# Optimization experiments

Hardware: AMD Instinct MI355X
Metric: run time of the kernel (lower is better)

## Reference

```python
import jax, jax.numpy as jnp
import numpy as np

DIM = 1024
NUM_HEADS = 16
HEAD_DIM = DIM // NUM_HEADS
B, T = 2, 2048


def _rope_tables(seq_len, head_dim, dtype=jnp.float32):
    inv_freq = 1.0 / (10000.0 ** (jnp.arange(0, head_dim, 2, dtype=jnp.float32) / head_dim))
    t = jnp.arange(seq_len, dtype=jnp.float32)
    freqs = jnp.einsum('i,j->ij', t, inv_freq)            # [T, head_dim/2]
    emb = jnp.concatenate((freqs, freqs), axis=-1)         # [T, head_dim]
    return jnp.cos(emb).astype(dtype), jnp.sin(emb).astype(dtype)


def _rotate_half(x):
    x1, x2 = x[..., : x.shape[-1] // 2], x[..., x.shape[-1] // 2 :]
    return jnp.concatenate((-x2, x1), axis=-1)


def setup_inputs() -> dict:
    key = jax.random.key(0)
    ks = jax.random.split(key, 5)
    s = 1.0 / np.sqrt(DIM)
    return {
        'x': jax.random.normal(ks[0], (B, T, DIM), dtype=jnp.float32),
        'w_q': jax.random.normal(ks[1], (DIM, DIM), dtype=jnp.float32) * s,
        'w_k': jax.random.normal(ks[2], (DIM, DIM), dtype=jnp.float32) * s,
        'w_v': jax.random.normal(ks[3], (DIM, DIM), dtype=jnp.float32) * s,
        'w_out': jax.random.normal(ks[4], (DIM, DIM), dtype=jnp.float32) * s,
    }


def reference(x, w_q, w_k, w_v, w_out):
    Bn, Tn, C = x.shape
    scale = HEAD_DIM ** -0.5
    # nn.Linear(bias=False): y = x @ W^T; reshape to [B, H, T, Dh]
    def proj(w):
        y = jnp.einsum('btc,dc->btd', x, w)
        return y.reshape(Bn, Tn, NUM_HEADS, HEAD_DIM).transpose(0, 2, 1, 3)
    q, k, v = proj(w_q), proj(w_k), proj(w_v)
    cos, sin = _rope_tables(Tn, HEAD_DIM, x.dtype)         # [T, Dh], broadcasts over B,H
    q = q * cos + _rotate_half(q) * sin
    k = k * cos + _rotate_half(k) * sin
    attn = jnp.einsum('bhqd,bhkd->bhqk', q, k) * scale     # [B,H,T,T]
    attn = jax.nn.softmax(attn, axis=-1)
    out = jnp.einsum('bhqk,bhkd->bhqd', attn, v)           # [B,H,T,Dh]
    out = out.transpose(0, 2, 1, 3).reshape(Bn, Tn, C)
    return jnp.einsum('btc,dc->btd', out, w_out)
```

## Files before the change

### kernel.cpp

```cpp
#include <hip/hip_runtime.h>


typedef _Float16 f16;
typedef f16 f16x8 __attribute__((ext_vector_type(8)));
typedef __fp16 fp16x2 __attribute__((ext_vector_type(2)));
typedef float f32x4 __attribute__((ext_vector_type(4)));
typedef float f32x16 __attribute__((ext_vector_type(16)));
typedef unsigned int u32;
typedef unsigned short u16;

union V16 { uint4 u; f16x8 h; };

__device__ __forceinline__ float exp2_fast(float x) {
#if __has_builtin(__builtin_amdgcn_exp2f)
  return __builtin_amdgcn_exp2f(x);
#else
  return __expf(x * 0.69314718056f);
#endif
}

__device__ __forceinline__ u32 pkrtz(float a, float b) {
  union { fp16x2 h; u32 u; } cv;
  cv.h = __builtin_amdgcn_cvt_pkrtz(a, b);
  return cv.u;
}

#define PLSWAP(a, b)                                                          \
  asm volatile("s_nop 1\n\tv_permlane32_swap_b32 %0, %1" : "+v"(a), "+v"(b))

#define GLDS(src, dst) __builtin_amdgcn_global_load_lds(                      \
    (const __attribute__((address_space(1))) void*)(const void*)(src),        \
    (__attribute__((address_space(3))) void*)(void*)(dst), 16, 0, 0)

__global__ __launch_bounds__(256) void rope_tables_kernel(float* __restrict__ cosT,
                                                          float* __restrict__ sinT) {
  int i = blockIdx.x * 256 + threadIdx.x;
  int t = i >> 5, j = i & 31;
  float inv = 1.0f / powf(10000.0f, (float)(2 * j) * (1.0f / 64.0f));
  float ang = (float)t * inv;
  double a = (double)ang;
  cosT[i] = (float)cos(a);
  sinT[i] = (float)sin(a);
}

__global__ __launch_bounds__(256)
void cvt5_kernel(const float* __restrict__ x,  const float* __restrict__ wq,
                 const float* __restrict__ wk, const float* __restrict__ wv,
                 const float* __restrict__ wo,
                 f16* __restrict__ xh, f16* __restrict__ W3,
                 f16* __restrict__ woh) {
  int bx = blockIdx.x;
  const float* src; f16* dst; int i;
  if (bx < 4096) {
    src = x; dst = xh; i = bx * 256 + threadIdx.x;
  } else {
    int b = (bx - 4096) >> 10;
    i = ((bx - 4096) & 1023) * 256 + threadIdx.x;
    src = (b == 0) ? wq : (b == 1) ? wk : (b == 2) ? wv : wo;
    dst = (b == 3) ? woh : W3 + (size_t)b * 1048576;
  }
  float4 v = ((const float4*)src)[i];
  union { f16 h[4]; uint2 u; } cv;
  cv.h[0] = (f16)v.x; cv.h[1] = (f16)v.y; cv.h[2] = (f16)v.z; cv.h[3] = (f16)v.w;
  ((uint2*)dst)[i] = cv.u;
}

__global__ __launch_bounds__(256)
void gemm_qkv_kernel(const f16* __restrict__ X,
                     const f16* __restrict__ W3,
                     f16* __restrict__ Qo, f16* __restrict__ Ko,
                     f16* __restrict__ VTo,
                     const float* __restrict__ cosT,
                     const float* __restrict__ sinT) {
  __shared__ u16 lds[2][8192];

  const int tid = threadIdx.x, lane = tid & 63, w = tid >> 6;
  const int c = lane & 15, g = lane >> 4;
  const int m0 = blockIdx.x * 128;
  const int by = blockIdx.y;
  const int wsel = by >> 3, hp = by & 7, h0 = hp * 2;
  const f16* Wb = W3 + (size_t)wsel * (1024 * 1024) + (size_t)hp * 128 * 1024;

  const int n1 = tid, n2 = tid + 256;
  const int r1 = n1 >> 2, gc1 = (n1 & 3) ^ ((n1 >> 3) & 3);
  const int r2 = n2 >> 2, gc2 = (n2 & 3) ^ ((n2 >> 3) & 3);
  const f16* gA1 = X + (size_t)(m0 + r1) * 1024 + gc1 * 8;
  const f16* gA2 = X + (size_t)(m0 + r2) * 1024 + gc2 * 8;
  const f16* gB1 = Wb + (size_t)r1 * 1024 + gc1 * 8;
  const f16* gB2 = Wb + (size_t)r2 * 1024 + gc2 * 8;
  const int dA1 = n1 * 8, dA2 = n2 * 8;
  const int dB1 = 4096 + n1 * 8, dB2 = 4096 + n2 * 8;

  f32x4 acc[2][8];
  const f32x4 zero = {0.f, 0.f, 0.f, 0.f};
#pragma unroll
  for (int mi = 0; mi < 2; ++mi)
#pragma unroll
    for (int ni = 0; ni < 8; ++ni) acc[mi][ni] = zero;

#define STAGE_QKV(buf, kt) do {                                               \
    const int ko = (kt) * 32;                                                 \
    GLDS(gA1 + ko, &lds[buf][dA1]);                                           \
    GLDS(gA2 + ko, &lds[buf][dA2]);                                           \
    GLDS(gB1 + ko, &lds[buf][dB1]);                                           \
    GLDS(gB2 + ko, &lds[buf][dB2]);                                           \
  } while (0)

  const int swz = (g ^ ((c >> 1) & 3)) * 8;

  STAGE_QKV(0, 0);
  __syncthreads();
  for (int kt = 0; kt < 32; ++kt) {
    const int cur = kt & 1;
    if (kt < 31) STAGE_QKV(cur ^ 1, kt + 1);
    V16 a[2], b[8];
#pragma unroll
    for (int mi = 0; mi < 2; ++mi)
      a[mi].u = *(const uint4*)&lds[cur][(w * 32 + mi * 16 + c) * 32 + swz];
#pragma unroll
    for (int ni = 0; ni < 8; ++ni)
      b[ni].u = *(const uint4*)&lds[cur][4096 + (ni * 16 + c) * 32 + swz];
    __builtin_amdgcn_s_setprio(1);
#pragma unroll
    for (int mi = 0; mi < 2; ++mi)
#pragma unroll
      for (int ni = 0; ni < 8; ++ni)
        acc[mi][ni] = __builtin_amdgcn_mfma_f32_16x16x32_f16(a[mi].h, b[ni].h, acc[mi][ni], 0, 0, 0);
    __builtin_amdgcn_s_setprio(0);
    __syncthreads();
  }

  if (wsel < 2) {
    f16* Out = (wsel == 0) ? Qo : Ko;
    const float psc = (wsel == 0) ? 0.18033688f : 1.0f;
#pragma unroll
    for (int mi = 0; mi < 2; ++mi)
#pragma unroll
      for (int r = 0; r < 4; ++r) {
        int m = m0 + w * 32 + mi * 16 + g * 4 + r;
        int bb = m >> 11, t = m & 2047;
        float co0 = cosT[t * 32 + c],      si0 = sinT[t * 32 + c];
        float co1 = cosT[t * 32 + 16 + c], si1 = sinT[t * 32 + 16 + c];
#pragma unroll
        for (int ni = 0; ni < 8; ++ni) {
          int head = h0 + (ni >> 2);
          int d = (ni & 3) * 16 + c;
          float co = (ni & 1) ? co1 : co0;
          float si = (ni & 1) ? si1 : si0;
          float partner = acc[mi][ni ^ 2][r];
          float v = (acc[mi][ni][r] * co + ((d < 32) ? -partner : partner) * si) * psc;
          Out[((size_t)(bb * 16 + head) * 2048 + t) * 64 + d] = (f16)v;
        }
      }
  } else {
    u16* sT = &lds[0][0];
    const int bbv = m0 >> 11;
    const int t0 = (m0 & 2047) + w * 32;
#pragma unroll
    for (int p = 0; p < 2; ++p) {
#pragma unroll
      for (int mi = 0; mi < 2; ++mi)
#pragma unroll
        for (int nn = 0; nn < 4; ++nn)
#pragma unroll
          for (int r = 0; r < 4; ++r) {
            int ni = p * 4 + nn;
            int dl = nn * 16 + c;
            int tl = mi * 16 + g * 4 + r;
            union { f16 h; u16 u; } cv; cv.h = (f16)acc[mi][ni][r];
            sT[w * 2560 + dl * 40 + tl] = cv.u;
          }
      f16* dst = VTo + ((size_t)(bbv * 16 + h0 + p) * 64 + lane) * 2048 + t0;
      const u16* srcp = &sT[w * 2560 + lane * 40];
      *(uint4*)(dst +  0) = *(const uint4*)(srcp +  0);
      *(uint4*)(dst +  8) = *(const uint4*)(srcp +  8);
      *(uint4*)(dst + 16) = *(const uint4*)(srcp + 16);
      *(uint4*)(dst + 24) = *(const uint4*)(srcp + 24);
    }
  }
}

__global__ __launch_bounds__(256)
void gemm_out_kernel(const f16* __restrict__ AH, const f16* __restrict__ BH,
                     float* __restrict__ outF) {
  __shared__ u16 lds[2][6144];

  const int tid = threadIdx.x, lane = tid & 63, w = tid >> 6;
  const int c = lane & 15, g = lane >> 4;
  const int m0 = blockIdx.x * 128, n0 = blockIdx.y * 64;

  const int n1 = tid, n2 = tid + 256;
  const int r1 = n1 >> 2, gc1 = (n1 & 3) ^ ((n1 >> 3) & 3);
  const int r2 = n2 >> 2, gc2 = (n2 & 3) ^ ((n2 >> 3) & 3);
  const f16* gA1 = AH + (size_t)(m0 + r1) * 1024 + gc1 * 8;
  const f16* gA2 = AH + (size_t)(m0 + r2) * 1024 + gc2 * 8;
  const f16* gB1 = BH + (size_t)(n0 + r1) * 1024 + gc1 * 8;
  const int dA1 = n1 * 8, dA2 = n2 * 8;
  const int dB1 = 4096 + n1 * 8;

  f32x4 acc[2][4];
  const f32x4 zero = {0.f, 0.f, 0.f, 0.f};
#pragma unroll
  for (int mi = 0; mi < 2; ++mi)
#pragma unroll
    for (int ni = 0; ni < 4; ++ni) acc[mi][ni] = zero;

#define STAGE_OUT(buf, kt) do {                                               \
    const int ko = (kt) * 32;                                                 \
    GLDS(gA1 + ko, &lds[buf][dA1]);                                           \
    GLDS(gA2 + ko, &lds[buf][dA2]);                                           \
    GLDS(gB1 + ko, &lds[buf][dB1]);                                           \
  } while (0)

  const int swz = (g ^ ((c >> 1) & 3)) * 8;

  STAGE_OUT(0, 0);
  __syncthreads();
  for (int kt = 0; kt < 32; ++kt) {
    const int cur = kt & 1;
    if (kt < 31) STAGE_OUT(cur ^ 1, kt + 1);
    V16 a[2], b[4];
#pragma unroll
    for (int mi = 0; mi < 2; ++mi)
      a[mi].u = *(const uint4*)&lds[cur][(w * 32 + mi * 16 + c) * 32 + swz];
#pragma unroll
    for (int ni = 0; ni < 4; ++ni)
      b[ni].u = *(const uint4*)&lds[cur][4096 + (ni * 16 + c) * 32 + swz];
    __builtin_amdgcn_s_setprio(1);
#pragma unroll
    for (int mi = 0; mi < 2; ++mi)
#pragma unroll
      for (int ni = 0; ni < 4; ++ni)
        acc[mi][ni] = __builtin_amdgcn_mfma_f32_16x16x32_f16(a[mi].h, b[ni].h, acc[mi][ni], 0, 0, 0);
    __builtin_amdgcn_s_setprio(0);
    __syncthreads();
  }

#pragma unroll
  for (int mi = 0; mi < 2; ++mi)
#pragma unroll
    for (int r = 0; r < 4; ++r) {
      int m = m0 + w * 32 + mi * 16 + g * 4 + r;
#pragma unroll
      for (int ni = 0; ni < 4; ++ni)
        outF[(size_t)m * 1024 + n0 + ni * 16 + c] = acc[mi][ni][r];
    }
}

__global__ __launch_bounds__(256, 2)
void attn_kernel(const f16* __restrict__ Q, const f16* __restrict__ K,
                 const f16* __restrict__ VT, f16* __restrict__ OH) {
  __shared__ u16 sKV[3][8192];
  __shared__ u16 sT16[4][32][36];

  const int tid = threadIdx.x, lane = tid & 63, wid = tid >> 6;
  const int q32 = lane & 31, hi = lane >> 5;
  const int bx = blockIdx.x;
  const int bh = (bx & 7) + 8 * (bx >> 7);
  const int qt = (bx >> 3) & 15;
  const int bb = bh >> 4, hh = bh & 15;
  const int q0 = qt * 128 + wid * 32;

  V16 qf[4];
  const f16* qp = Q + ((size_t)bh * 2048 + q0 + q32) * 64 + 8 * hi;
#pragma unroll
  for (int kd = 0; kd < 4; ++kd)
    qf[kd].u = *(const uint4*)(qp + 16 * kd);

  f32x16 o0 = 0.0f, o1 = 0.0f;
  float lsum = 0.f;

  const int srow = tid >> 3, scol = tid & 7;
  const f16* gK = K  + ((size_t)bh * 2048 + srow) * 64 + scol * 8;
  const f16* gV = VT + ((size_t)bh * 64 + srow) * 2048 + scol * 8;
  const int dst0 = srow * 128 + ((scol ^ (srow & 7)) << 4);
  const int dst1 = dst0 + 32 * 128;

  uint4 rk0, rk1, rv0, rv1;
#define LOADT(kt) do {                                                        \
    const f16* pk = gK + (size_t)(kt) * 4096;                                 \
    rk0 = *(const uint4*)(pk);                                                \
    rk1 = *(const uint4*)(pk + 32 * 64);                                      \
    const f16* pv = gV + (size_t)(kt) * 64;                                   \
    rv0 = *(const uint4*)(pv);                                                \
    rv1 = *(const uint4*)(pv + 32 * 2048);                                    \
  } while (0)
#define WRITET(buf) do {                                                      \
    char* base_ = (char*)&sKV[buf][0];                                        \
    *(uint4*)(base_ + dst0) = rk0; *(uint4*)(base_ + dst1) = rk1;             \
    *(uint4*)(base_ + 8192 + dst0) = rv0; *(uint4*)(base_ + 8192 + dst1) = rv1;\
  } while (0)

  const int swzrow = (q32 & 7) << 4;

#define QKT(D0, D1, buf) do {                                                 \
    D0 = 0.0f; D1 = 0.0f;                                                     \
    const char* kb_ = (const char*)&sKV[buf][0];                              \
    __builtin_amdgcn_s_setprio(1);                                            \
    _Pragma("unroll")                                                         \
    for (int kd = 0; kd < 4; ++kd) {                                          \
      const int off = ((32 * kd + 16 * hi) ^ swzrow);                         \
      V16 kf0, kf1;                                                           \
      kf0.u = *(const uint4*)(kb_ + q32 * 128 + off);                         \
      kf1.u = *(const uint4*)(kb_ + (32 + q32) * 128 + off);                  \
      D0 = __builtin_amdgcn_mfma_f32_32x32x16_f16(kf0.h, qf[kd].h, D0, 0, 0, 0);\
      D1 = __builtin_amdgcn_mfma_f32_32x32x16_f16(kf1.h, qf[kd].h, D1, 0, 0, 0);\
    }                                                                         \
    __builtin_amdgcn_s_setprio(0);                                            \
  } while (0)

#define SOFTMAX_PB() do {                                                     \
    u32 c0[8], c1[8];                                                         \
    _Pragma("unroll")                                                         \
    for (int m = 0; m < 8; ++m) {                                             \
      float p0 = exp2_fast(st0[2 * m]);                                       \
      float p1 = exp2_fast(st0[2 * m + 1]);                                   \
      lsum += p0 + p1; c0[m] = pkrtz(p0, p1);                                 \
      float p2 = exp2_fast(st1[2 * m]);                                       \
      float p3 = exp2_fast(st1[2 * m + 1]);                                   \
      lsum += p2 + p3; c1[m] = pkrtz(p2, p3);                                 \
    }                                                                         \
    { u32 y0 = c0[0], x0 = c0[2]; PLSWAP(y0, x0);                             \
      u32 y1 = c0[1], x1 = c0[3]; PLSWAP(y1, x1);                             \
      pB[0].u.x = y0; pB[0].u.y = y1; pB[0].u.z = x0; pB[0].u.w = x1;         \
      u32 y2 = c0[4], x2 = c0[6]; PLSWAP(y2, x2);                             \
      u32 y3 = c0[5], x3 = c0[7]; PLSWAP(y3, x3);                             \
      pB[1].u.x = y2; pB[1].u.y = y3; pB[1].u.z = x2; pB[1].u.w = x3;         \
      u32 y4 = c1[0], x4 = c1[2]; PLSWAP(y4, x4);                             \
      u32 y5 = c1[1], x5 = c1[3]; PLSWAP(y5, x5);                             \
      pB[2].u.x = y4; pB[2].u.y = y5; pB[2].u.z = x4; pB[2].u.w = x5;         \
      u32 y6 = c1[4], x6 = c1[6]; PLSWAP(y6, x6);                             \
      u32 y7 = c1[5], x7 = c1[7]; PLSWAP(y7, x7);                             \
      pB[3].u.x = y6; pB[3].u.y = y7; pB[3].u.z = x6; pB[3].u.w = x7; }       \
  } while (0)

#define PVOP(buf) do {                                                        \
    const char* vb_ = (const char*)&sKV[buf][0] + 8192;                       \
    __builtin_amdgcn_s_setprio(1);                                            \
    _Pragma("unroll")                                                         \
    for (int ks = 0; ks < 4; ++ks) {                                          \
      const int off = ((32 * ks + 16 * hi) ^ swzrow);                         \
      V16 vf0, vf1;                                                           \
      vf0.u = *(const uint4*)(vb_ + q32 * 128 + off);                         \
      vf1.u = *(const uint4*)(vb_ + (32 + q32) * 128 + off);                  \
      o0 = __builtin_amdgcn_mfma_f32_32x32x16_f16(vf0.h, pB[ks].h, o0, 0, 0, 0);\
      o1 = __builtin_amdgcn_mfma_f32_32x32x16_f16(vf1.h, pB[ks].h, o1, 0, 0, 0);\
    }                                                                         \
    __builtin_amdgcn_s_setprio(0);                                            \
  } while (0)

  LOADT(0);
  WRITET(0);
  __syncthreads();
  LOADT(1);
  f32x16 st0, st1;
  QKT(st0, st1, 0);

  V16 pB[4];
  int bw = 1, bp = 0;
  for (int kt = 0; kt < 31; ++kt) {
    WRITET(bw);
    __syncthreads();
    if (kt < 30) LOADT(kt + 2);
    SOFTMAX_PB();
    QKT(st0, st1, bw);
    PVOP(bp);
    bp = bw; bw = (bw == 2) ? 0 : bw + 1;
  }
  SOFTMAX_PB();
  PVOP(bp);

  const float l_run = lsum + __shfl_xor(lsum, 32, 64);
  const float inv = 1.0f / l_run;
  const int qr = lane >> 1, dh = (lane & 1) * 16;
#pragma unroll
  for (int dt = 0; dt < 2; ++dt) {
#pragma unroll
    for (int r = 0; r < 16; ++r) {
      float v = (dt ? o1[r] : o0[r]) * inv;
      union { f16 h; u16 u; } cv; cv.h = (f16)v;
      sT16[wid][q32][(r & 3) + 8 * (r >> 2) + 4 * hi] = cv.u;
    }
    __syncthreads();
    const u16* sp = &sT16[wid][qr][dh];
    uint2 a0 = *(const uint2*)(sp + 0),  a1 = *(const uint2*)(sp + 4);
    uint2 a2 = *(const uint2*)(sp + 8),  a3 = *(const uint2*)(sp + 12);
    size_t gbase = ((size_t)bb * 2048 + q0 + qr) * 1024 + hh * 64 + 32 * dt + dh;
    *(uint2*)(OH + gbase + 0)  = a0;
    *(uint2*)(OH + gbase + 4)  = a1;
    *(uint2*)(OH + gbase + 8)  = a2;
    *(uint2*)(OH + gbase + 12) = a3;
    __syncthreads();
  }
}

extern "C" void kernel_launch(void* const* d_in, const int* in_sizes, int n_in,
                              void* d_out, int out_size, void* d_ws, size_t ws_size,
                              hipStream_t stream) {
  const float* x  = (const float*)d_in[0];
  const float* wq = (const float*)d_in[1];
  const float* wk = (const float*)d_in[2];
  const float* wv = (const float*)d_in[3];
  const float* wo = (const float*)d_in[4];

  constexpr size_t SZ_X   = 4096ull * 1024 * 2;
  constexpr size_t SZ_W   = 1024ull * 1024 * 2;
  constexpr size_t SZ_QKV = 2ull * 16 * 2048 * 64 * 2;
  constexpr size_t SZ_TBL = 2048ull * 32 * 4;
  constexpr size_t NEED = SZ_X + 4 * SZ_W + 3 * SZ_QKV + 2 * SZ_TBL;
  if (ws_size < NEED) return;

  char* ws = (char*)d_ws;
  f16* xh  = (f16*)(ws);
  f16* W3  = (f16*)(ws + SZ_X);
  f16* woh = (f16*)(ws + SZ_X + 3 * SZ_W);
  char* p  = ws + SZ_X + 4 * SZ_W;
  f16* qb  = (f16*)(p);            p += SZ_QKV;
  f16* kb  = (f16*)(p);            p += SZ_QKV;
  f16* vT  = (f16*)(p);            p += SZ_QKV;
  float* cosT = (float*)(p);       p += SZ_TBL;
  float* sinT = (float*)(p);
  f16* oh = xh;

  rope_tables_kernel<<<256, 256, 0, stream>>>(cosT, sinT);
  cvt5_kernel<<<8192, 256, 0, stream>>>(x, wq, wk, wv, wo, xh, W3, woh);

  gemm_qkv_kernel<<<dim3(32, 24), 256, 0, stream>>>(xh, W3, qb, kb, vT,
                                                    cosT, sinT);

  attn_kernel<<<512, 256, 0, stream>>>(qb, kb, vT, oh);

  gemm_out_kernel<<<dim3(32, 16), 256, 0, stream>>>(oh, woh, (float*)d_out);
}
```

Measured before the change: 130.4 us.

## Triple-buffer GEMM pipelines with 2x2 warp tiling and larger output tile

Both GEMM kernels move from double-buffered to triple-buffered LDS staging with a prefetch distance of two tiles. They wait with explicit vmcnt waits plus barriers instead of a full __syncthreads drain. Warps are rearranged into a 2x2 grid of 64x64 sub-tiles, which cuts LDS fragment reads per MFMA. The output GEMM tile grows from 128x64 to 128x128, halving its grid. The V-transpose epilogue is rewritten for the new layout. The cost is more LDS per block and possibly fewer blocks for the output GEMM to spread over CUs.

New measurement: 120.1 us. 1.09x faster.

```diff
diff --git a/kernel.cpp b/kernel.cpp
--- a/kernel.cpp
+++ b/kernel.cpp
@@ -31,6 +31,12 @@
 #define GLDS(src, dst) __builtin_amdgcn_global_load_lds(                      \
     (const __attribute__((address_space(1))) void*)(const void*)(src),        \
     (__attribute__((address_space(3))) void*)(void*)(dst), 16, 0, 0)
+
+#define WAITBAR(N) do {                                                       \
+    asm volatile("s_waitcnt vmcnt(" #N ")" ::: "memory");                     \
+    __builtin_amdgcn_s_barrier();                                             \
+    __builtin_amdgcn_sched_barrier(0);                                        \
+  } while (0)
 
 __global__ __launch_bounds__(256) void rope_tables_kernel(float* __restrict__ cosT,
                                                           float* __restrict__ sinT) {
@@ -72,9 +78,10 @@
                      f16* __restrict__ VTo,
                      const float* __restrict__ cosT,
                      const float* __restrict__ sinT) {
-  __shared__ u16 lds[2][8192];
+  __shared__ u16 lds[3][8192];
 
   const int tid = threadIdx.x, lane = tid & 63, w = tid >> 6;
+  const int wr = w >> 1, wc = w & 1;
   const int c = lane & 15, g = lane >> 4;
   const int m0 = blockIdx.x * 128;
   const int by = blockIdx.y;
@@ -91,12 +98,12 @@
   const int dA1 = n1 * 8, dA2 = n2 * 8;
   const int dB1 = 4096 + n1 * 8, dB2 = 4096 + n2 * 8;
 
-  f32x4 acc[2][8];
+  f32x4 acc[4][4];
   const f32x4 zero = {0.f, 0.f, 0.f, 0.f};
 #pragma unroll
-  for (int mi = 0; mi < 2; ++mi)
-#pragma unroll
-    for (int ni = 0; ni < 8; ++ni) acc[mi][ni] = zero;
+  for (int mi = 0; mi < 4; ++mi)
+#pragma unroll
+    for (int ni = 0; ni < 4; ++ni) acc[mi][ni] = zero;
 
 #define STAGE_QKV(buf, kt) do {                                               \
     const int ko = (kt) * 32;                                                 \
@@ -109,42 +116,46 @@
   const int swz = (g ^ ((c >> 1) & 3)) * 8;
 
   STAGE_QKV(0, 0);
-  __syncthreads();
+  STAGE_QKV(1, 1);
+  WAITBAR(4);
+
+  int cur = 0, nx2 = 2;
   for (int kt = 0; kt < 32; ++kt) {
-    const int cur = kt & 1;
-    if (kt < 31) STAGE_QKV(cur ^ 1, kt + 1);
-    V16 a[2], b[8];
-#pragma unroll
-    for (int mi = 0; mi < 2; ++mi)
-      a[mi].u = *(const uint4*)&lds[cur][(w * 32 + mi * 16 + c) * 32 + swz];
-#pragma unroll
-    for (int ni = 0; ni < 8; ++ni)
-      b[ni].u = *(const uint4*)&lds[cur][4096 + (ni * 16 + c) * 32 + swz];
+    if (kt < 30) STAGE_QKV(nx2, kt + 2);
+    V16 a[4], b[4];
+#pragma unroll
+    for (int mi = 0; mi < 4; ++mi)
+      a[mi].u = *(const uint4*)&lds[cur][(wr * 64 + mi * 16 + c) * 32 + swz];
+#pragma unroll
+    for (int ni = 0; ni < 4; ++ni)
+      b[ni].u = *(const uint4*)&lds[cur][4096 + (wc * 64 + ni * 16 + c) * 32 + swz];
     __builtin_amdgcn_s_setprio(1);
 #pragma unroll
-    for (int mi = 0; mi < 2; ++mi)
-#pragma unroll
-      for (int ni = 0; ni < 8; ++ni)
+    for (int mi = 0; mi < 4; ++mi)
+#pragma unroll
+      for (int ni = 0; ni < 4; ++ni)
         acc[mi][ni] = __builtin_amdgcn_mfma_f32_16x16x32_f16(a[mi].h, b[ni].h, acc[mi][ni], 0, 0, 0);
     __builtin_amdgcn_s_setprio(0);
-    __syncthreads();
+    if (kt < 30) WAITBAR(4); else WAITBAR(0);
+    cur = (cur == 2) ? 0 : cur + 1;
+    nx2 = (nx2 == 2) ? 0 : nx2 + 1;
   }
 
   if (wsel < 2) {
     f16* Out = (wsel == 0) ? Qo : Ko;
     const float psc = (wsel == 0) ? 0.18033688f : 1.0f;
-#pragma unroll
-    for (int mi = 0; mi < 2; ++mi)
+    const int head = h0 + wc;
+#pragma unroll
+    for (int mi = 0; mi < 4; ++mi)
 #pragma unroll
       for (int r = 0; r < 4; ++r) {
-        int m = m0 + w * 32 + mi * 16 + g * 4 + r;
+        int m = m0 + wr * 64 + mi * 16 + g * 4 + r;
         int bb = m >> 11, t = m & 2047;
         float co0 = cosT[t * 32 + c],      si0 = sinT[t * 32 + c];
         float co1 = cosT[t * 32 + 16 + c], si1 = sinT[t * 32 + 16 + c];
 #pragma unroll
-        for (int ni = 0; ni < 8; ++ni) {
-          int head = h0 + (ni >> 2);
-          int d = (ni & 3) * 16 + c;
+        for (int ni = 0; ni < 4; ++ni) {
+          int d = ni * 16 + c;
           float co = (ni & 1) ? co1 : co0;
           float si = (ni & 1) ? si1 : si0;
           float partner = acc[mi][ni ^ 2][r];
@@ -154,40 +165,37 @@
       }
   } else {
     u16* sT = &lds[0][0];
+    const int head = h0 + wc;
     const int bbv = m0 >> 11;
-    const int t0 = (m0 & 2047) + w * 32;
-#pragma unroll
-    for (int p = 0; p < 2; ++p) {
-#pragma unroll
-      for (int mi = 0; mi < 2; ++mi)
-#pragma unroll
-        for (int nn = 0; nn < 4; ++nn)
-#pragma unroll
-          for (int r = 0; r < 4; ++r) {
-            int ni = p * 4 + nn;
-            int dl = nn * 16 + c;
-            int tl = mi * 16 + g * 4 + r;
-            union { f16 h; u16 u; } cv; cv.h = (f16)acc[mi][ni][r];
-            sT[w * 2560 + dl * 40 + tl] = cv.u;
-          }
-      f16* dst = VTo + ((size_t)(bbv * 16 + h0 + p) * 64 + lane) * 2048 + t0;
-      const u16* srcp = &sT[w * 2560 + lane * 40];
-      *(uint4*)(dst +  0) = *(const uint4*)(srcp +  0);
-      *(uint4*)(dst +  8) = *(const uint4*)(srcp +  8);
-      *(uint4*)(dst + 16) = *(const uint4*)(srcp + 16);
-      *(uint4*)(dst + 24) = *(const uint4*)(srcp + 24);
-    }
+    const int t0 = (m0 & 2047) + wr * 64;
+#pragma unroll
+    for (int mi = 0; mi < 4; ++mi)
+#pragma unroll
+      for (int ni = 0; ni < 4; ++ni)
+#pragma unroll
+        for (int r = 0; r < 4; ++r) {
+          int dl = ni * 16 + c;
+          int tl = mi * 16 + g * 4 + r;
+          union { f16 h; u16 u; } cv; cv.h = (f16)acc[mi][ni][r];
+          sT[w * 4608 + dl * 72 + tl] = cv.u;
+        }
+    f16* dst = VTo + ((size_t)(bbv * 16 + head) * 64 + lane) * 2048 + t0;
+    const u16* srcp = &sT[w * 4608 + lane * 72];
+#pragma unroll
+    for (int s = 0; s < 16; ++s)
+      *(uint2*)(dst + s * 4) = *(const uint2*)(srcp + s * 4);
   }
 }
 
 __global__ __launch_bounds__(256)
 void gemm_out_kernel(const f16* __restrict__ AH, const f16* __restrict__ BH,
                      float* __restrict__ outF) {
-  __shared__ u16 lds[2][6144];
+  __shared__ u16 lds[3][8192];
 
   const int tid = threadIdx.x, lane = tid & 63, w = tid >> 6;
+  const int wr = w >> 1, wc = w & 1;
   const int c = lane & 15, g = lane >> 4;
-  const int m0 = blockIdx.x * 128, n0 = blockIdx.y * 64;
+  const int m0 = blockIdx.x * 128, n0 = blockIdx.y * 128;
 
   const int n1 = tid, n2 = tid + 256;
   const int r1 = n1 >> 2, gc1 = (n1 & 3) ^ ((n1 >> 3) & 3);
@@ -195,13 +203,14 @@
   const f16* gA1 = AH + (size_t)(m0 + r1) * 1024 + gc1 * 8;
   const f16* gA2 = AH + (size_t)(m0 + r2) * 1024 + gc2 * 8;
   const f16* gB1 = BH + (size_t)(n0 + r1) * 1024 + gc1 * 8;
+  const f16* gB2 = BH + (size_t)(n0 + r2) * 1024 + gc2 * 8;
   const int dA1 = n1 * 8, dA2 = n2 * 8;
-  const int dB1 = 4096 + n1 * 8;
-
-  f32x4 acc[2][4];
+  const int dB1 = 4096 + n1 * 8, dB2 = 4096 + n2 * 8;
+
+  f32x4 acc[4][4];
   const f32x4 zero = {0.f, 0.f, 0.f, 0.f};
 #pragma unroll
-  for (int mi = 0; mi < 2; ++mi)
+  for (int mi = 0; mi < 4; ++mi)
 #pragma unroll
     for (int ni = 0; ni < 4; ++ni) acc[mi][ni] = zero;
 
@@ -210,40 +219,45 @@
     GLDS(gA1 + ko, &lds[buf][dA1]);                                           \
     GLDS(gA2 + ko, &lds[buf][dA2]);                                           \
     GLDS(gB1 + ko, &lds[buf][dB1]);                                           \
+    GLDS(gB2 + ko, &lds[buf][dB2]);                                           \
   } while (0)
 
   const int swz = (g ^ ((c >> 1) & 3)) * 8;
 
   STAGE_OUT(0, 0);
-  __syncthreads();
+  STAGE_OUT(1, 1);
+  WAITBAR(4);
+
+  int cur = 0, nx2 = 2;
   for (int kt = 0; kt < 32; ++kt) {
-    const int cur = kt & 1;
-    if (kt < 31) STAGE_OUT(cur ^ 1, kt + 1);
-    V16 a[2], b[4];
-#pragma unroll
-    for (int mi = 0; mi < 2; ++mi)
-      a[mi].u = *(const uint4*)&lds[cur][(w * 32 + mi * 16 + c) * 32 + swz];
+    if (kt < 30) STAGE_OUT(nx2, kt + 2);
+    V16 a[4], b[4];
+#pragma unroll
+    for (int mi = 0; mi < 4; ++mi)
+      a[mi].u = *(const uint4*)&lds[cur][(wr * 64 + mi * 16 + c) * 32 + swz];
 #pragma unroll
     for (int ni = 0; ni < 4; ++ni)
-      b[ni].u = *(const uint4*)&lds[cur][4096 + (ni * 16 + c) * 32 + swz];
+      b[ni].u = *(const uint4*)&lds[cur][4096 + (wc * 64 + ni * 16 + c) * 32 + swz];
     __builtin_amdgcn_s_setprio(1);
 #pragma unroll
-    for (int mi = 0; mi < 2; ++mi)
+    for (int mi = 0; mi < 4; ++mi)
 #pragma unroll
       for (int ni = 0; ni < 4; ++ni)
         acc[mi][ni] = __builtin_amdgcn_mfma_f32_16x16x32_f16(a[mi].h, b[ni].h, acc[mi][ni], 0, 0, 0);
     __builtin_amdgcn_s_setprio(0);
-    __syncthreads();
-  }
-
-#pragma unroll
-  for (int mi = 0; mi < 2; ++mi)
+    if (kt < 30) WAITBAR(4); else WAITBAR(0);
+    cur = (cur == 2) ? 0 : cur + 1;
+    nx2 = (nx2 == 2) ? 0 : nx2 + 1;
+  }
+
+#pragma unroll
+  for (int mi = 0; mi < 4; ++mi)
 #pragma unroll
     for (int r = 0; r < 4; ++r) {
-      int m = m0 + w * 32 + mi * 16 + g * 4 + r;
+      int m = m0 + wr * 64 + mi * 16 + g * 4 + r;
 #pragma unroll
       for (int ni = 0; ni < 4; ++ni)
-        outF[(size_t)m * 1024 + n0 + ni * 16 + c] = acc[mi][ni][r];
+        outF[(size_t)m * 1024 + n0 + wc * 64 + ni * 16 + c] = acc[mi][ni][r];
     }
 }
 
@@ -430,5 +444,5 @@
 
   attn_kernel<<<512, 256, 0, stream>>>(qb, kb, vT, oh);
 
-  gemm_out_kernel<<<dim3(32, 16), 256, 0, stream>>>(oh, woh, (float*)d_out);
-}
+  gemm_out_kernel<<<dim3(32, 8), 256, 0, stream>>>(oh, woh, (float*)d_out);
+}
```
